# Performance work log

Hardware: AMD Instinct MI355X
Metric: run time of the kernel (lower is better)

The kernel has to match this reference:

```python
import jax, jax.numpy as jnp
import numpy as np

B, N, DIN, DM, NH = 8, 2048, 256, 256, 4
DK = DM // NH


def setup_inputs() -> dict:
    key = jax.random.key(0)
    ks = jax.random.split(key, 8)
    x = jax.random.normal(ks[0], (B, N, DIN), dtype=jnp.float32)
    # contiguous valid ranges per sample (padding on both ends), matching
    # the module's assumption that torch.where(mask)[0][0]/[−1] define a span
    starts = jax.random.randint(ks[1], (B,), 0, N // 8)
    lens = jax.random.randint(ks[2], (B,), N // 2, N - N // 8)
    pos = jnp.arange(N)
    attention_mask = ((pos[None, :] >= starts[:, None])
                      & (pos[None, :] < starts[:, None] + lens[:, None])).astype(jnp.int32)
    s = 0.02
    Wq = jax.random.normal(ks[3], (DIN, DM), jnp.float32) * s
    Wk = jax.random.normal(ks[4], (DIN, DM), jnp.float32) * s
    Wv = jax.random.normal(ks[5], (DIN, DM), jnp.float32) * s
    Wo = jax.random.normal(ks[6], (DM, DM), jnp.float32) * s
    bq = jnp.zeros((DM,), jnp.float32)
    bk = jnp.zeros((DM,), jnp.float32)
    bv = jnp.zeros((DM,), jnp.float32)
    bo = jnp.zeros((DM,), jnp.float32)
    return {"x": x, "attention_mask": attention_mask,
            "Wq": Wq, "bq": bq, "Wk": Wk, "bk": bk,
            "Wv": Wv, "bv": bv, "Wo": Wo, "bo": bo}


def reference(x, attention_mask, Wq, bq, Wk, bk, Wv, bv, Wo, bo):
    b, n, _ = x.shape
    nh, dk = NH, DK
    scale = 1.0 / np.sqrt(dk)
    q = (x @ Wq + bq).reshape(b, n, nh, dk).transpose(0, 2, 1, 3)  # [b,h,n,dk]
    k = (x @ Wk + bk).reshape(b, n, nh, dk).transpose(0, 2, 1, 3)
    v = (x @ Wv + bv).reshape(b, n, nh, dk).transpose(0, 2, 1, 3)
    dist = jnp.einsum('bhid,bhjd->bhij', q, k) * scale  # [b,h,n,n]

    # Vectorized equivalent of the per-sample python-loop mask:
    # start = first True index; end = last True index (torch slice start:end
    # is EXCLUSIVE of the last valid position -- preserved faithfully).
    m = attention_mask.astype(bool)
    pos = jnp.arange(n)
    start = jnp.argmax(m, axis=1)                      # [b]
    end = n - 1 - jnp.argmax(m[:, ::-1], axis=1)       # [b] last True index
    valid = (pos[None, :] >= start[:, None]) & (pos[None, :] < end[:, None])  # [b,n]
    bias = jnp.where(valid[:, :, None] & valid[:, None, :], 0.0, -1e10)       # [b,n,n]

    dist = jax.nn.softmax(dist + bias[:, None, :, :], axis=-1)
    att = jnp.einsum('bhij,bhjd->bhid', dist, v)       # [b,h,n,dk]
    att = att.transpose(0, 2, 1, 3).reshape(b, n, nh * dk)
    return att @ Wo + bo
```

## Files before the change

kernel.cpp:

```cpp
#include <hip/hip_runtime.h>
#include <hip/hip_bf16.h>
#include <math.h>

namespace {
constexpr int Bb  = 8;
constexpr int Nn  = 2048;
constexpr int DIN_ = 256;
constexpr int DM_  = 256;
constexpr int NH_  = 4;
constexpr int DK_  = 64;
constexpr int BH_  = Bb * NH_;
constexpr float SCALE = 0.125f;
}

typedef __attribute__((ext_vector_type(8))) _Float16 half8;
typedef __attribute__((ext_vector_type(2))) __fp16 fp16x2;
typedef __attribute__((ext_vector_type(4))) float f32x4;

static __device__ __forceinline__ unsigned pkrtz_u32(float a, float b) {
    union { fp16x2 h; unsigned u; } u;
    u.h = __builtin_amdgcn_cvt_pkrtz(a, b);
    return u.u;
}

static __device__ __forceinline__ half8 h8_from_u32x4(unsigned w0, unsigned w1,
                                                      unsigned w2, unsigned w3) {
    union { unsigned u[4]; half8 h; } u;
    u.u[0] = w0; u.u[1] = w1; u.u[2] = w2; u.u[3] = w3;
    return u.h;
}

__global__ __launch_bounds__(256) void prep_kernel(
    const int* __restrict__ mask, int* __restrict__ bounds,
    const float* __restrict__ x, _Float16* __restrict__ xh,
    const float* __restrict__ W0, const float* __restrict__ W1,
    const float* __restrict__ W2, const float* __restrict__ W3,
    _Float16* __restrict__ T0, _Float16* __restrict__ T1,
    _Float16* __restrict__ T2, _Float16* __restrict__ T3)
{
    const int bid = blockIdx.x;
    const int tid = threadIdx.x;
    if (bid < 8) {
        const int b = bid;
        __shared__ int smin[256], smax[256];
        int lmin = Nn, lmax = -1;
        for (int i = tid; i < Nn; i += 256) {
            if (mask[b * Nn + i]) {
                if (i < lmin) lmin = i;
                if (i > lmax) lmax = i;
            }
        }
        smin[tid] = lmin; smax[tid] = lmax;
        __syncthreads();
        for (int s = 128; s > 0; s >>= 1) {
            if (tid < s) {
                smin[tid] = min(smin[tid], smin[tid + s]);
                smax[tid] = max(smax[tid], smax[tid + s]);
            }
            __syncthreads();
        }
        if (tid == 0) { bounds[b * 2] = smin[0]; bounds[b * 2 + 1] = smax[0]; }
    } else if (bid < 8 + 2048) {
        const size_t i = ((size_t)(bid - 8) * 256 + tid) * 8;
        float4 v0 = *(const float4*)&x[i];
        float4 v1 = *(const float4*)&x[i + 4];
        _Float16 h[8];
        h[0]=(_Float16)v0.x; h[1]=(_Float16)v0.y; h[2]=(_Float16)v0.z; h[3]=(_Float16)v0.w;
        h[4]=(_Float16)v1.x; h[5]=(_Float16)v1.y; h[6]=(_Float16)v1.z; h[7]=(_Float16)v1.w;
        *(uint4*)&xh[i] = *(const uint4*)h;
    } else {
        const int lin = bid - 2056;
        const int wsel = lin >> 6;
        const float* W; _Float16* T;
        switch (wsel) {
            case 0: W = W0; T = T0; break;
            case 1: W = W1; T = T1; break;
            case 2: W = W2; T = T2; break;
            default: W = W3; T = T3; break;
        }
        const int idx = (lin & 63) * 256 + tid;
        const int n = idx & 255;
        const int k0 = (idx >> 8) << 2;
        _Float16 h4[4];
        #pragma unroll
        for (int j = 0; j < 4; ++j) h4[j] = (_Float16)W[(size_t)(k0 + j) * 256 + n];
        *(uint2*)&T[(size_t)n * 256 + k0] = *(const uint2*)h4;
    }
}

__global__ __launch_bounds__(256) void qkv_mfma(
    const _Float16* __restrict__ xh,
    const _Float16* __restrict__ Wtq, const float* __restrict__ bq,
    const _Float16* __restrict__ Wtk, const float* __restrict__ bk,
    const _Float16* __restrict__ Wtv, const float* __restrict__ bv,
    _Float16* __restrict__ Qh, _Float16* __restrict__ Kh, _Float16* __restrict__ Vt)
{
    const int z = blockIdx.z;
    const _Float16* Wt; const float* bias;
    if (z == 0)      { Wt = Wtq; bias = bq; }
    else if (z == 1) { Wt = Wtk; bias = bk; }
    else             { Wt = Wtv; bias = bv; }

    const int m0 = blockIdx.x * 128;
    const int n0 = blockIdx.y * 64;
    const int tid = threadIdx.x;
    const int w = tid >> 6, lane = tid & 63;
    const int a = lane & 15, g = lane >> 4;
    const int mb = m0 + 32 * w;

    f32x4 d0[4] = {{0,0,0,0},{0,0,0,0},{0,0,0,0},{0,0,0,0}};
    f32x4 d1[4] = {{0,0,0,0},{0,0,0,0},{0,0,0,0},{0,0,0,0}};

    const _Float16* A0 = xh + (size_t)(mb + a) * 256 + 8 * g;
    const _Float16* A1 = xh + (size_t)(mb + 16 + a) * 256 + 8 * g;
    const _Float16* Wr0 = Wt + (size_t)(n0 +  0 + a) * 256 + 8 * g;
    const _Float16* Wr1 = Wt + (size_t)(n0 + 16 + a) * 256 + 8 * g;
    const _Float16* Wr2 = Wt + (size_t)(n0 + 32 + a) * 256 + 8 * g;
    const _Float16* Wr3 = Wt + (size_t)(n0 + 48 + a) * 256 + 8 * g;

    #pragma unroll
    for (int kc = 0; kc < 8; ++kc) {
        const half8 af0 = *(const half8*)(A0 + 32 * kc);
        const half8 af1 = *(const half8*)(A1 + 32 * kc);
        const half8 b0 = *(const half8*)(Wr0 + 32 * kc);
        const half8 b1 = *(const half8*)(Wr1 + 32 * kc);
        const half8 b2 = *(const half8*)(Wr2 + 32 * kc);
        const half8 b3 = *(const half8*)(Wr3 + 32 * kc);
        d0[0] = __builtin_amdgcn_mfma_f32_16x16x32_f16(af0, b0, d0[0], 0,0,0);
        d1[0] = __builtin_amdgcn_mfma_f32_16x16x32_f16(af1, b0, d1[0], 0,0,0);
        d0[1] = __builtin_amdgcn_mfma_f32_16x16x32_f16(af0, b1, d0[1], 0,0,0);
        d1[1] = __builtin_amdgcn_mfma_f32_16x16x32_f16(af1, b1, d1[1], 0,0,0);
        d0[2] = __builtin_amdgcn_mfma_f32_16x16x32_f16(af0, b2, d0[2], 0,0,0);
        d1[2] = __builtin_amdgcn_mfma_f32_16x16x32_f16(af1, b2, d1[2], 0,0,0);
        d0[3] = __builtin_amdgcn_mfma_f32_16x16x32_f16(af0, b3, d0[3], 0,0,0);
        d1[3] = __builtin_amdgcn_mfma_f32_16x16x32_f16(af1, b3, d1[3], 0,0,0);
    }

    #pragma unroll
    for (int t = 0; t < 2; ++t) {
        const int mrow = mb + 16 * t + 4 * g;
        #pragma unroll
        for (int nf = 0; nf < 4; ++nf) {
            const f32x4 dv = t == 0 ? d0[nf] : d1[nf];
            const int n = n0 + 16 * nf + a;
            const float bs = bias[n];
            const int bh = (mrow >> 11) * NH_ + (n >> 6);
            const int dk = n & 63;
            if (z < 2) {
                _Float16* out = z ? Kh : Qh;
                #pragma unroll
                for (int r = 0; r < 4; ++r) {
                    const int tok = (mrow + r) & 2047;
                    out[((size_t)bh * Nn + tok) * DK_ + dk] = (_Float16)(dv[r] + bs);
                }
            } else {
                const int tok = mrow & 2047;
                uint2 pk;
                pk.x = pkrtz_u32(dv[0] + bs, dv[1] + bs);
                pk.y = pkrtz_u32(dv[2] + bs, dv[3] + bs);
                *(uint2*)&Vt[((size_t)bh * DK_ + dk) * Nn + tok] = pk;
            }
        }
    }
}

__global__ __launch_bounds__(256) void colmean_kernel(const _Float16* __restrict__ Vt,
                                                      float* __restrict__ cm) {
    const int bh = blockIdx.x;
    const int t = threadIdx.x;
    const int d = t >> 2, part = t & 3;
    const _Float16* src = Vt + ((size_t)bh * DK_ + d) * Nn + part * 512;
    float s = 0.f;
    for (int i = 0; i < 512; i += 8) {
        half8 v = *(const half8*)(src + i);
        #pragma unroll
        for (int j = 0; j < 8; ++j) s += (float)v[j];
    }
    __shared__ float red[64][4];
    red[d][part] = s;
    __syncthreads();
    if (part == 0)
        cm[bh * DK_ + d] = (red[d][0] + red[d][1] + red[d][2] + red[d][3]) * (1.0f / 2048.0f);
}

__global__ __launch_bounds__(256) void flash_mfma(
    const _Float16* __restrict__ Q, const _Float16* __restrict__ K,
    const _Float16* __restrict__ Vt, const int* __restrict__ bounds,
    const float* __restrict__ cm, _Float16* __restrict__ att)
{
    const int bid = blockIdx.x;
    const int xcd = bid & 7;
    const int rest = bid >> 3;
    const int qb  = rest & 31;
    const int bh  = (xcd << 2) | (rest >> 5);
    const int b  = bh >> 2, h = bh & 3;
    const int q0 = qb * 64;
    const int tid  = threadIdx.x;
    const int w    = tid >> 6;
    const int lane = tid & 63;
    const int a = lane & 15, g = lane >> 4;
    const int start = bounds[2 * b], endv = bounds[2 * b + 1];

    __shared__ __align__(16) _Float16 kfr[2][8][512];
    __shared__ __align__(16) _Float16 vfr[2][8][512];

    const float* cmb = cm + bh * DK_;
    _Float16* attb = att + ((size_t)b * Nn) * DM_ + h * DK_;

    if (q0 + 63 < start || q0 >= endv) {
        #pragma unroll
        for (int td = 0; td < 4; ++td) {
            const _Float16 cmv = (_Float16)cmb[16 * td + a];
            #pragma unroll
            for (int r = 0; r < 4; ++r) {
                const int qr = q0 + 16 * w + 4 * g + r;
                attb[(size_t)qr * DM_ + 16 * td + a] = cmv;
            }
        }
        return;
    }

    const _Float16* Qb = Q  + (size_t)bh * Nn * DK_;
    const _Float16* Kb = K  + (size_t)bh * Nn * DK_;
    const _Float16* Vb = Vt + (size_t)bh * DK_ * Nn;

    const int qrow = q0 + 16 * w + a;
    const half8 qf0 = *(const half8*)&Qb[(size_t)qrow * DK_ + 8 * g];
    const half8 qf1 = *(const half8*)&Qb[(size_t)qrow * DK_ + 32 + 8 * g];

    float l_i = 0.0f;
    f32x4 o0 = {0.f,0.f,0.f,0.f}, o1 = {0.f,0.f,0.f,0.f};
    f32x4 o2 = {0.f,0.f,0.f,0.f}, o3 = {0.f,0.f,0.f,0.f};

#define STAGE(cbuf, kt_) do {                                                        \
        _Pragma("unroll")                                                            \
        for (int ff = 0; ff < 2; ++ff) {                                             \
            const int f  = 2 * w + ff;                                               \
            const int tt = f >> 1, cc = f & 1;                                       \
            const _Float16* ks = &Kb[(size_t)((kt_) + 16 * tt + a) * DK_ + 32 * cc + 8 * g]; \
            __builtin_amdgcn_global_load_lds(                                        \
                (const __attribute__((address_space(1))) void*)ks,                   \
                (__attribute__((address_space(3))) void*)&kfr[cbuf][f][0], 16, 0, 0);\
            const _Float16* vs = &Vb[(size_t)(16 * tt + a) * Nn + (kt_) + 32 * cc + 8 * g]; \
            __builtin_amdgcn_global_load_lds(                                        \
                (const __attribute__((address_space(1))) void*)vs,                   \
                (__attribute__((address_space(3))) void*)&vfr[cbuf][f][0], 16, 0, 0);\
        }                                                                            \
    } while (0)

    const int lo = (start >> 6) * 64;
    int c = 0;
    STAGE(0, lo);

    for (int kt = lo; kt < endv; kt += 64) {
        const int nxt = kt + 64;
        if (nxt < endv) {
            STAGE(c ^ 1, nxt);
            asm volatile("s_waitcnt vmcnt(4)" ::: "memory");
        } else {
            asm volatile("s_waitcnt vmcnt(0)" ::: "memory");
        }
        __builtin_amdgcn_s_barrier();

        const _Float16* kf = &kfr[c][0][0];
        const _Float16* vf = &vfr[c][0][0];

        f32x4 st0 = {0.f,0.f,0.f,0.f}, st1 = {0.f,0.f,0.f,0.f};
        f32x4 st2 = {0.f,0.f,0.f,0.f}, st3 = {0.f,0.f,0.f,0.f};
        st0 = __builtin_amdgcn_mfma_f32_16x16x32_f16(*(const half8*)&kf[0*512 + lane*8], qf0, st0, 0,0,0);
        st0 = __builtin_amdgcn_mfma_f32_16x16x32_f16(*(const half8*)&kf[1*512 + lane*8], qf1, st0, 0,0,0);
        st1 = __builtin_amdgcn_mfma_f32_16x16x32_f16(*(const half8*)&kf[2*512 + lane*8], qf0, st1, 0,0,0);
        st1 = __builtin_amdgcn_mfma_f32_16x16x32_f16(*(const half8*)&kf[3*512 + lane*8], qf1, st1, 0,0,0);
        st2 = __builtin_amdgcn_mfma_f32_16x16x32_f16(*(const half8*)&kf[4*512 + lane*8], qf0, st2, 0,0,0);
        st2 = __builtin_amdgcn_mfma_f32_16x16x32_f16(*(const half8*)&kf[5*512 + lane*8], qf1, st2, 0,0,0);
        st3 = __builtin_amdgcn_mfma_f32_16x16x32_f16(*(const half8*)&kf[6*512 + lane*8], qf0, st3, 0,0,0);
        st3 = __builtin_amdgcn_mfma_f32_16x16x32_f16(*(const half8*)&kf[7*512 + lane*8], qf1, st3, 0,0,0);

        float pv[4][4];
        float rsum = 0.0f;
        const bool edge = (kt < start) || (kt + 64 > endv);
        if (edge) {
            #pragma unroll
            for (int t = 0; t < 4; ++t) {
                const f32x4 sv = (t == 0) ? st0 : (t == 1) ? st1 : (t == 2) ? st2 : st3;
                #pragma unroll
                for (int r = 0; r < 4; ++r) {
                    const int col = kt + 16 * t + 4 * g + r;
                    const bool ok = (col >= start) && (col < endv);
                    const float e = ok ? __expf(sv[r] * SCALE) : 0.0f;
                    pv[t][r] = e;
                    rsum += e;
                }
            }
        } else {
            #pragma unroll
            for (int t = 0; t < 4; ++t) {
                const f32x4 sv = (t == 0) ? st0 : (t == 1) ? st1 : (t == 2) ? st2 : st3;
                #pragma unroll
                for (int r = 0; r < 4; ++r) {
                    const float e = __expf(sv[r] * SCALE);
                    pv[t][r] = e;
                    rsum += e;
                }
            }
        }
        rsum += __shfl_xor(rsum, 16, 64);
        rsum += __shfl_xor(rsum, 32, 64);
        l_i += rsum;

        unsigned pk[4][2];
        #pragma unroll
        for (int t = 0; t < 4; ++t) {
            pk[t][0] = pkrtz_u32(pv[t][0], pv[t][1]);
            pk[t][1] = pkrtz_u32(pv[t][2], pv[t][3]);
        }
        const int gsel = g >> 1;
        unsigned aw[2][4];
        #pragma unroll
        for (int cq = 0; cq < 2; ++cq) {
            #pragma unroll
            for (int wd = 0; wd < 4; ++wd) {
                const int srcLane = a + 16 * (2 * (g & 1) + (wd >> 1));
                const int lo2 = __shfl((int)pk[2 * cq    ][wd & 1], srcLane, 64);
                const int hi2 = __shfl((int)pk[2 * cq + 1][wd & 1], srcLane, 64);
                aw[cq][wd] = (unsigned)(gsel ? hi2 : lo2);
            }
        }
        const half8 pa0 = h8_from_u32x4(aw[0][0], aw[0][1], aw[0][2], aw[0][3]);
        const half8 pa1 = h8_from_u32x4(aw[1][0], aw[1][1], aw[1][2], aw[1][3]);

        o0 = __builtin_amdgcn_mfma_f32_16x16x32_f16(pa0, *(const half8*)&vf[0*512 + lane*8], o0, 0,0,0);
        o0 = __builtin_amdgcn_mfma_f32_16x16x32_f16(pa1, *(const half8*)&vf[1*512 + lane*8], o0, 0,0,0);
        o1 = __builtin_amdgcn_mfma_f32_16x16x32_f16(pa0, *(const half8*)&vf[2*512 + lane*8], o1, 0,0,0);
        o1 = __builtin_amdgcn_mfma_f32_16x16x32_f16(pa1, *(const half8*)&vf[3*512 + lane*8], o1, 0,0,0);
        o2 = __builtin_amdgcn_mfma_f32_16x16x32_f16(pa0, *(const half8*)&vf[4*512 + lane*8], o2, 0,0,0);
        o2 = __builtin_amdgcn_mfma_f32_16x16x32_f16(pa1, *(const half8*)&vf[5*512 + lane*8], o2, 0,0,0);
        o3 = __builtin_amdgcn_mfma_f32_16x16x32_f16(pa0, *(const half8*)&vf[6*512 + lane*8], o3, 0,0,0);
        o3 = __builtin_amdgcn_mfma_f32_16x16x32_f16(pa1, *(const half8*)&vf[7*512 + lane*8], o3, 0,0,0);

        asm volatile("" ::: "memory");
        __builtin_amdgcn_s_barrier();
        c ^= 1;
    }
#undef STAGE

    const float inv = 1.0f / l_i;
    const float ir0 = __shfl(inv, 4 * g + 0, 64);
    const float ir1 = __shfl(inv, 4 * g + 1, 64);
    const float ir2 = __shfl(inv, 4 * g + 2, 64);
    const float ir3 = __shfl(inv, 4 * g + 3, 64);

    #pragma unroll
    for (int td = 0; td < 4; ++td) {
        const f32x4 ov = (td == 0) ? o0 : (td == 1) ? o1 : (td == 2) ? o2 : o3;
        const float cmv = cmb[16 * td + a];
        const float irs[4] = {ir0, ir1, ir2, ir3};
        #pragma unroll
        for (int r = 0; r < 4; ++r) {
            const int qr = q0 + 16 * w + 4 * g + r;
            const bool valid = (qr >= start) && (qr < endv);
            const float val = valid ? ov[r] * irs[r] : cmv;
            attb[(size_t)qr * DM_ + 16 * td + a] = (_Float16)val;
        }
    }
}

__global__ __launch_bounds__(256) void proj_mfma(
    const _Float16* __restrict__ A, const _Float16* __restrict__ Wt,
    const float* __restrict__ bias, float* __restrict__ out)
{
    const int m0 = blockIdx.x * 128;
    const int n0 = blockIdx.y * 64;
    const int tid = threadIdx.x;
    const int w = tid >> 6, lane = tid & 63;
    const int a = lane & 15, g = lane >> 4;
    const int mb = m0 + 32 * w;

    f32x4 d0[4] = {{0,0,0,0},{0,0,0,0},{0,0,0,0},{0,0,0,0}};
    f32x4 d1[4] = {{0,0,0,0},{0,0,0,0},{0,0,0,0},{0,0,0,0}};

    const _Float16* A0 = A + (size_t)(mb + a) * 256 + 8 * g;
    const _Float16* A1 = A + (size_t)(mb + 16 + a) * 256 + 8 * g;
    const _Float16* Wr0 = Wt + (size_t)(n0 +  0 + a) * 256 + 8 * g;
    const _Float16* Wr1 = Wt + (size_t)(n0 + 16 + a) * 256 + 8 * g;
    const _Float16* Wr2 = Wt + (size_t)(n0 + 32 + a) * 256 + 8 * g;
    const _Float16* Wr3 = Wt + (size_t)(n0 + 48 + a) * 256 + 8 * g;

    #pragma unroll
    for (int kc = 0; kc < 8; ++kc) {
        const half8 af0 = *(const half8*)(A0 + 32 * kc);
        const half8 af1 = *(const half8*)(A1 + 32 * kc);
        const half8 b0 = *(const half8*)(Wr0 + 32 * kc);
        const half8 b1 = *(const half8*)(Wr1 + 32 * kc);
        const half8 b2 = *(const half8*)(Wr2 + 32 * kc);
        const half8 b3 = *(const half8*)(Wr3 + 32 * kc);
        d0[0] = __builtin_amdgcn_mfma_f32_16x16x32_f16(af0, b0, d0[0], 0,0,0);
        d1[0] = __builtin_amdgcn_mfma_f32_16x16x32_f16(af1, b0, d1[0], 0,0,0);
        d0[1] = __builtin_amdgcn_mfma_f32_16x16x32_f16(af0, b1, d0[1], 0,0,0);
        d1[1] = __builtin_amdgcn_mfma_f32_16x16x32_f16(af1, b1, d1[1], 0,0,0);
        d0[2] = __builtin_amdgcn_mfma_f32_16x16x32_f16(af0, b2, d0[2], 0,0,0);
        d1[2] = __builtin_amdgcn_mfma_f32_16x16x32_f16(af1, b2, d1[2], 0,0,0);
        d0[3] = __builtin_amdgcn_mfma_f32_16x16x32_f16(af0, b3, d0[3], 0,0,0);
        d1[3] = __builtin_amdgcn_mfma_f32_16x16x32_f16(af1, b3, d1[3], 0,0,0);
    }

    #pragma unroll
    for (int t = 0; t < 2; ++t) {
        const int mrow = mb + 16 * t + 4 * g;
        #pragma unroll
        for (int nf = 0; nf < 4; ++nf) {
            const f32x4 dv = t == 0 ? d0[nf] : d1[nf];
            const int n = n0 + 16 * nf + a;
            const float bs = bias[n];
            #pragma unroll
            for (int r = 0; r < 4; ++r)
                out[(size_t)(mrow + r) * DM_ + n] = dv[r] + bs;
        }
    }
}

extern "C" void kernel_launch(void* const* d_in, const int* in_sizes, int n_in,
                              void* d_out, int out_size, void* d_ws, size_t ws_size,
                              hipStream_t stream)
{
    const float* x    = (const float*)d_in[0];
    const int*   mask = (const int*)d_in[1];
    const float* Wq   = (const float*)d_in[2];
    const float* bq   = (const float*)d_in[3];
    const float* Wk   = (const float*)d_in[4];
    const float* bk   = (const float*)d_in[5];
    const float* Wv   = (const float*)d_in[6];
    const float* bv   = (const float*)d_in[7];
    const float* Wo   = (const float*)d_in[8];
    const float* bo   = (const float*)d_in[9];
    float* out = (float*)d_out;

    char* ws = (char*)d_ws;
    size_t off = 0;
    int* bounds = (int*)ws;                 off += 256;
    float* cmv  = (float*)(ws + off);       off += (size_t)BH_ * DK_ * sizeof(float);
    off = (off + 255) & ~(size_t)255;
    const size_t h16_bytes = (size_t)BH_ * Nn * DK_ * sizeof(_Float16);
    _Float16* xh  = (_Float16*)(ws + off); off += h16_bytes;
    _Float16* Qh  = (_Float16*)(ws + off); off += h16_bytes;
    _Float16* Kh  = (_Float16*)(ws + off); off += h16_bytes;
    _Float16* Vt  = (_Float16*)(ws + off); off += h16_bytes;
    _Float16* ath = (_Float16*)(ws + off); off += h16_bytes;
    _Float16* Wtq = (_Float16*)(ws + off); off += 256 * 256 * sizeof(_Float16);
    _Float16* Wtk = (_Float16*)(ws + off); off += 256 * 256 * sizeof(_Float16);
    _Float16* Wtv = (_Float16*)(ws + off); off += 256 * 256 * sizeof(_Float16);
    _Float16* Wto = (_Float16*)(ws + off); off += 256 * 256 * sizeof(_Float16);

    prep_kernel<<<2312, 256, 0, stream>>>(mask, bounds, x, xh,
                                          Wq, Wk, Wv, Wo, Wtq, Wtk, Wtv, Wto);

    dim3 g1(Bb * Nn / 128, DM_ / 64, 3);
    qkv_mfma<<<g1, 256, 0, stream>>>(xh, Wtq, bq, Wtk, bk, Wtv, bv, Qh, Kh, Vt);

    colmean_kernel<<<BH_, 256, 0, stream>>>(Vt, cmv);

    flash_mfma<<<1024, 256, 0, stream>>>(Qh, Kh, Vt, bounds, cmv, ath);

    dim3 g3(Bb * Nn / 128, DM_ / 64);
    proj_mfma<<<g3, 256, 0, stream>>>(ath, Wto, bo, out);
}
```

Measured before the change: 208.9 us.

## Split attention key range in two and merge partial results in combine kernel

Flash attention now splits each query block's key range into two halves handled by separate workgroups, doubling the grid. Each writes unnormalised fp16 partial outputs and row sums, and a new combine kernel adds them, normalises, and fills padded rows with the column mean. The goal is more parallelism and better load balance across CUs. The cost is an extra kernel launch and the extra global traffic for the partial buffers. It also risks lower precision, since unnormalised partial sums are stored in fp16.

```diff
diff --git a/kernel.cpp b/kernel.cpp
--- a/kernel.cpp
+++ b/kernel.cpp
@@ -186,13 +186,15 @@
 __global__ __launch_bounds__(256) void flash_mfma(
     const _Float16* __restrict__ Q, const _Float16* __restrict__ K,
     const _Float16* __restrict__ Vt, const int* __restrict__ bounds,
-    const float* __restrict__ cm, _Float16* __restrict__ att)
+    _Float16* __restrict__ Oh, float* __restrict__ lw)
 {
     const int bid = blockIdx.x;
     const int xcd = bid & 7;
     const int rest = bid >> 3;
     const int qb  = rest & 31;
-    const int bh  = (xcd << 2) | (rest >> 5);
+    const int j   = (rest >> 5) & 3;
+    const int s   = rest >> 7;
+    const int bh  = j * 8 + xcd;
     const int b  = bh >> 2, h = bh & 3;
     const int q0 = qb * 64;
     const int tid  = threadIdx.x;
@@ -201,24 +203,10 @@
     const int a = lane & 15, g = lane >> 4;
     const int start = bounds[2 * b], endv = bounds[2 * b + 1];
 
+    if (q0 + 63 < start || q0 >= endv) return;
+
     __shared__ __align__(16) _Float16 kfr[2][8][512];
     __shared__ __align__(16) _Float16 vfr[2][8][512];
-
-    const float* cmb = cm + bh * DK_;
-    _Float16* attb = att + ((size_t)b * Nn) * DM_ + h * DK_;
-
-    if (q0 + 63 < start || q0 >= endv) {
-        #pragma unroll
-        for (int td = 0; td < 4; ++td) {
-            const _Float16 cmv = (_Float16)cmb[16 * td + a];
-            #pragma unroll
-            for (int r = 0; r < 4; ++r) {
-                const int qr = q0 + 16 * w + 4 * g + r;
-                attb[(size_t)qr * DM_ + 16 * td + a] = cmv;
-            }
-        }
-        return;
-    }
 
     const _Float16* Qb = Q  + (size_t)bh * Nn * DK_;
     const _Float16* Kb = K  + (size_t)bh * Nn * DK_;
@@ -248,120 +236,167 @@
         }                                                                            \
     } while (0)
 
-    const int lo = (start >> 6) * 64;
-    int c = 0;
-    STAGE(0, lo);
-
-    for (int kt = lo; kt < endv; kt += 64) {
-        const int nxt = kt + 64;
-        if (nxt < endv) {
-            STAGE(c ^ 1, nxt);
-            asm volatile("s_waitcnt vmcnt(4)" ::: "memory");
-        } else {
-            asm volatile("s_waitcnt vmcnt(0)" ::: "memory");
-        }
-        __builtin_amdgcn_s_barrier();
-
-        const _Float16* kf = &kfr[c][0][0];
-        const _Float16* vf = &vfr[c][0][0];
-
-        f32x4 st0 = {0.f,0.f,0.f,0.f}, st1 = {0.f,0.f,0.f,0.f};
-        f32x4 st2 = {0.f,0.f,0.f,0.f}, st3 = {0.f,0.f,0.f,0.f};
-        st0 = __builtin_amdgcn_mfma_f32_16x16x32_f16(*(const half8*)&kf[0*512 + lane*8], qf0, st0, 0,0,0);
-        st0 = __builtin_amdgcn_mfma_f32_16x16x32_f16(*(const half8*)&kf[1*512 + lane*8], qf1, st0, 0,0,0);
-        st1 = __builtin_amdgcn_mfma_f32_16x16x32_f16(*(const half8*)&kf[2*512 + lane*8], qf0, st1, 0,0,0);
-        st1 = __builtin_amdgcn_mfma_f32_16x16x32_f16(*(const half8*)&kf[3*512 + lane*8], qf1, st1, 0,0,0);
-        st2 = __builtin_amdgcn_mfma_f32_16x16x32_f16(*(const half8*)&kf[4*512 + lane*8], qf0, st2, 0,0,0);
-        st2 = __builtin_amdgcn_mfma_f32_16x16x32_f16(*(const half8*)&kf[5*512 + lane*8], qf1, st2, 0,0,0);
-        st3 = __builtin_amdgcn_mfma_f32_16x16x32_f16(*(const half8*)&kf[6*512 + lane*8], qf0, st3, 0,0,0);
-        st3 = __builtin_amdgcn_mfma_f32_16x16x32_f16(*(const half8*)&kf[7*512 + lane*8], qf1, st3, 0,0,0);
-
-        float pv[4][4];
-        float rsum = 0.0f;
-        const bool edge = (kt < start) || (kt + 64 > endv);
-        if (edge) {
+    const int t0 = start >> 6, t1 = (endv + 63) >> 6;
+    const int nt = t1 - t0;
+    const int n0t = (nt + 1) >> 1;
+    const int ts = (s == 0) ? t0 : t0 + n0t;
+    const int te = (s == 0) ? t0 + n0t : t1;
+
+    if (ts < te) {
+        const int lo = ts * 64, hiend = te * 64;
+        int c = 0;
+        STAGE(0, lo);
+
+        for (int kt = lo; kt < hiend; kt += 64) {
+            const int nxt = kt + 64;
+            if (nxt < hiend) {
+                STAGE(c ^ 1, nxt);
+                asm volatile("s_waitcnt vmcnt(4)" ::: "memory");
+            } else {
+                asm volatile("s_waitcnt vmcnt(0)" ::: "memory");
+            }
+            __builtin_amdgcn_s_barrier();
+
+            const _Float16* kf = &kfr[c][0][0];
+            const _Float16* vf = &vfr[c][0][0];
+
+            f32x4 st0 = {0.f,0.f,0.f,0.f}, st1 = {0.f,0.f,0.f,0.f};
+            f32x4 st2 = {0.f,0.f,0.f,0.f}, st3 = {0.f,0.f,0.f,0.f};
+            st0 = __builtin_amdgcn_mfma_f32_16x16x32_f16(*(const half8*)&kf[0*512 + lane*8], qf0, st0, 0,0,0);
+            st0 = __builtin_amdgcn_mfma_f32_16x16x32_f16(*(const half8*)&kf[1*512 + lane*8], qf1, st0, 0,0,0);
+            st1 = __builtin_amdgcn_mfma_f32_16x16x32_f16(*(const half8*)&kf[2*512 + lane*8], qf0, st1, 0,0,0);
+            st1 = __builtin_amdgcn_mfma_f32_16x16x32_f16(*(const half8*)&kf[3*512 + lane*8], qf1, st1, 0,0,0);
+            st2 = __builtin_amdgcn_mfma_f32_16x16x32_f16(*(const half8*)&kf[4*512 + lane*8], qf0, st2, 0,0,0);
+            st2 = __builtin_amdgcn_mfma_f32_16x16x32_f16(*(const half8*)&kf[5*512 + lane*8], qf1, st2, 0,0,0);
+            st3 = __builtin_amdgcn_mfma_f32_16x16x32_f16(*(const half8*)&kf[6*512 + lane*8], qf0, st3, 0,0,0);
+            st3 = __builtin_amdgcn_mfma_f32_16x16x32_f16(*(const half8*)&kf[7*512 + lane*8], qf1, st3, 0,0,0);
+
+            float pv[4][4];
+            float rsum = 0.0f;
+            const bool edge = (kt < start) || (kt + 64 > endv);
+            if (edge) {
+                #pragma unroll
+                for (int t = 0; t < 4; ++t) {
+                    const f32x4 sv = (t == 0) ? st0 : (t == 1) ? st1 : (t == 2) ? st2 : st3;
+                    #pragma unroll
+                    for (int r = 0; r < 4; ++r) {
+                        const int col = kt + 16 * t + 4 * g + r;
+                        const bool ok = (col >= start) && (col < endv);
+                        const float e = ok ? __expf(sv[r] * SCALE) : 0.0f;
+                        pv[t][r] = e;
+                        rsum += e;
+                    }
+                }
+            } else {
+                #pragma unroll
+                for (int t = 0; t < 4; ++t) {
+                    const f32x4 sv = (t == 0) ? st0 : (t == 1) ? st1 : (t == 2) ? st2 : st3;
+                    #pragma unroll
+                    for (int r = 0; r < 4; ++r) {
+                        const float e = __expf(sv[r] * SCALE);
+                        pv[t][r] = e;
+                        rsum += e;
+                    }
+                }
+            }
+            rsum += __shfl_xor(rsum, 16, 64);
+            rsum += __shfl_xor(rsum, 32, 64);
+            l_i += rsum;
+
+            unsigned pk[4][2];
             #pragma unroll
             for (int t = 0; t < 4; ++t) {
-                const f32x4 sv = (t == 0) ? st0 : (t == 1) ? st1 : (t == 2) ? st2 : st3;
+                pk[t][0] = pkrtz_u32(pv[t][0], pv[t][1]);
+                pk[t][1] = pkrtz_u32(pv[t][2], pv[t][3]);
+            }
+            const int gsel = g >> 1;
+            unsigned aw[2][4];
+            #pragma unroll
+            for (int cq = 0; cq < 2; ++cq) {
                 #pragma unroll
-                for (int r = 0; r < 4; ++r) {
-                    const int col = kt + 16 * t + 4 * g + r;
-                    const bool ok = (col >= start) && (col < endv);
-                    const float e = ok ? __expf(sv[r] * SCALE) : 0.0f;
-                    pv[t][r] = e;
-                    rsum += e;
+                for (int wd = 0; wd < 4; ++wd) {
+                    const int srcLane = a + 16 * (2 * (g & 1) + (wd >> 1));
+                    const int lo2 = __shfl((int)pk[2 * cq    ][wd & 1], srcLane, 64);
+                    const int hi2 = __shfl((int)pk[2 * cq + 1][wd & 1], srcLane, 64);
+                    aw[cq][wd] = (unsigned)(gsel ? hi2 : lo2);
                 }
             }
-        } else {
-            #pragma unroll
-            for (int t = 0; t < 4; ++t) {
-                const f32x4 sv = (t == 0) ? st0 : (t == 1) ? st1 : (t == 2) ? st2 : st3;
-                #pragma unroll
-                for (int r = 0; r < 4; ++r) {
-                    const float e = __expf(sv[r] * SCALE);
-                    pv[t][r] = e;
-                    rsum += e;
-                }
-            }
-        }
-        rsum += __shfl_xor(rsum, 16, 64);
-        rsum += __shfl_xor(rsum, 32, 64);
-        l_i += rsum;
-
-        unsigned pk[4][2];
-        #pragma unroll
-        for (int t = 0; t < 4; ++t) {
-            pk[t][0] = pkrtz_u32(pv[t][0], pv[t][1]);
-            pk[t][1] = pkrtz_u32(pv[t][2], pv[t][3]);
-        }
-        const int gsel = g >> 1;
-        unsigned aw[2][4];
-        #pragma unroll
-        for (int cq = 0; cq < 2; ++cq) {
-            #pragma unroll
-            for (int wd = 0; wd < 4; ++wd) {
-                const int srcLane = a + 16 * (2 * (g & 1) + (wd >> 1));
-                const int lo2 = __shfl((int)pk[2 * cq    ][wd & 1], srcLane, 64);
-                const int hi2 = __shfl((int)pk[2 * cq + 1][wd & 1], srcLane, 64);
-                aw[cq][wd] = (unsigned)(gsel ? hi2 : lo2);
-            }
-        }
-        const half8 pa0 = h8_from_u32x4(aw[0][0], aw[0][1], aw[0][2], aw[0][3]);
-        const half8 pa1 = h8_from_u32x4(aw[1][0], aw[1][1], aw[1][2], aw[1][3]);
-
-        o0 = __builtin_amdgcn_mfma_f32_16x16x32_f16(pa0, *(const half8*)&vf[0*512 + lane*8], o0, 0,0,0);
-        o0 = __builtin_amdgcn_mfma_f32_16x16x32_f16(pa1, *(const half8*)&vf[1*512 + lane*8], o0, 0,0,0);
-        o1 = __builtin_amdgcn_mfma_f32_16x16x32_f16(pa0, *(const half8*)&vf[2*512 + lane*8], o1, 0,0,0);
-        o1 = __builtin_amdgcn_mfma_f32_16x16x32_f16(pa1, *(const half8*)&vf[3*512 + lane*8], o1, 0,0,0);
-        o2 = __builtin_amdgcn_mfma_f32_16x16x32_f16(pa0, *(const half8*)&vf[4*512 + lane*8], o2, 0,0,0);
-        o2 = __builtin_amdgcn_mfma_f32_16x16x32_f16(pa1, *(const half8*)&vf[5*512 + lane*8], o2, 0,0,0);
-        o3 = __builtin_amdgcn_mfma_f32_16x16x32_f16(pa0, *(const half8*)&vf[6*512 + lane*8], o3, 0,0,0);
-        o3 = __builtin_amdgcn_mfma_f32_16x16x32_f16(pa1, *(const half8*)&vf[7*512 + lane*8], o3, 0,0,0);
-
-        asm volatile("" ::: "memory");
-        __builtin_amdgcn_s_barrier();
-        c ^= 1;
+            const half8 pa0 = h8_from_u32x4(aw[0][0], aw[0][1], aw[0][2], aw[0][3]);
+            const half8 pa1 = h8_from_u32x4(aw[1][0], aw[1][1], aw[1][2], aw[1][3]);
+
+            o0 = __builtin_amdgcn_mfma_f32_16x16x32_f16(pa0, *(const half8*)&vf[0*512 + lane*8], o0, 0,0,0);
+            o0 = __builtin_amdgcn_mfma_f32_16x16x32_f16(pa1, *(const half8*)&vf[1*512 + lane*8], o0, 0,0,0);
+            o1 = __builtin_amdgcn_mfma_f32_16x16x32_f16(pa0, *(const half8*)&vf[2*512 + lane*8], o1, 0,0,0);
+            o1 = __builtin_amdgcn_mfma_f32_16x16x32_f16(pa1, *(const half8*)&vf[3*512 + lane*8], o1, 0,0,0);
+            o2 = __builtin_amdgcn_mfma_f32_16x16x32_f16(pa0, *(const half8*)&vf[4*512 + lane*8], o2, 0,0,0);
+            o2 = __builtin_amdgcn_mfma_f32_16x16x32_f16(pa1, *(const half8*)&vf[5*512 + lane*8], o2, 0,0,0);
+            o3 = __builtin_amdgcn_mfma_f32_16x16x32_f16(pa0, *(const half8*)&vf[6*512 + lane*8], o3, 0,0,0);
+            o3 = __builtin_amdgcn_mfma_f32_16x16x32_f16(pa1, *(const half8*)&vf[7*512 + lane*8], o3, 0,0,0);
+
+            asm volatile("" ::: "memory");
+            __builtin_amdgcn_s_barrier();
+            c ^= 1;
+        }
     }
 #undef STAGE
 
-    const float inv = 1.0f / l_i;
-    const float ir0 = __shfl(inv, 4 * g + 0, 64);
-    const float ir1 = __shfl(inv, 4 * g + 1, 64);
-    const float ir2 = __shfl(inv, 4 * g + 2, 64);
-    const float ir3 = __shfl(inv, 4 * g + 3, 64);
-
+    const size_t half = (size_t)Bb * Nn * DM_;
+    _Float16* ob = Oh + (size_t)s * half + ((size_t)b * Nn) * DM_ + h * DK_;
     #pragma unroll
     for (int td = 0; td < 4; ++td) {
         const f32x4 ov = (td == 0) ? o0 : (td == 1) ? o1 : (td == 2) ? o2 : o3;
-        const float cmv = cmb[16 * td + a];
-        const float irs[4] = {ir0, ir1, ir2, ir3};
         #pragma unroll
         for (int r = 0; r < 4; ++r) {
             const int qr = q0 + 16 * w + 4 * g + r;
-            const bool valid = (qr >= start) && (qr < endv);
-            const float val = valid ? ov[r] * irs[r] : cmv;
-            attb[(size_t)qr * DM_ + 16 * td + a] = (_Float16)val;
-        }
+            ob[(size_t)qr * DM_ + 16 * td + a] = (_Float16)ov[r];
+        }
+    }
+    if (g == 0) {
+        const int tok = q0 + 16 * w + a;
+        lw[(size_t)s * BH_ * Nn + (size_t)bh * Nn + tok] = l_i;
+    }
+}
+
+__global__ __launch_bounds__(256) void combine_kernel(
+    const _Float16* __restrict__ Oh, const float* __restrict__ lw,
+    const int* __restrict__ bounds, const float* __restrict__ cm,
+    _Float16* __restrict__ att)
+{
+    const int b  = blockIdx.y;
+    const int q0 = blockIdx.x * 64;
+    const int t  = threadIdx.x;
+    const int row = q0 + (t >> 2);
+    const int h   = t & 3;
+    const int c0  = h * 64;
+    const int start = bounds[2 * b], endv = bounds[2 * b + 1];
+    const bool valid = (row >= start) && (row < endv);
+
+    const size_t half = (size_t)Bb * Nn * DM_;
+    const size_t rowoff = ((size_t)b * Nn + row) * DM_ + c0;
+
+    float inv = 0.0f;
+    if (valid) {
+        const int bh = b * NH_ + h;
+        const float l0 = lw[(size_t)bh * Nn + row];
+        const float l1 = lw[(size_t)BH_ * Nn + (size_t)bh * Nn + row];
+        inv = 1.0f / (l0 + l1);
+    }
+
+    #pragma unroll
+    for (int jj = 0; jj < 64; jj += 8) {
+        _Float16 o[8];
+        if (valid) {
+            half8 a0 = *(const half8*)&Oh[rowoff + jj];
+            half8 a1 = *(const half8*)&Oh[half + rowoff + jj];
+            #pragma unroll
+            for (int k = 0; k < 8; ++k)
+                o[k] = (_Float16)(((float)a0[k] + (float)a1[k]) * inv);
+        } else {
+            #pragma unroll
+            for (int k = 0; k < 8; ++k)
+                o[k] = (_Float16)cm[b * DM_ + c0 + jj + k];
+        }
+        *(uint4*)&att[rowoff + jj] = *(const uint4*)o;
     }
 }
 
@@ -440,11 +475,13 @@
     int* bounds = (int*)ws;                 off += 256;
     float* cmv  = (float*)(ws + off);       off += (size_t)BH_ * DK_ * sizeof(float);
     off = (off + 255) & ~(size_t)255;
+    float* lw   = (float*)(ws + off);       off += (size_t)2 * BH_ * Nn * sizeof(float);
     const size_t h16_bytes = (size_t)BH_ * Nn * DK_ * sizeof(_Float16);
     _Float16* xh  = (_Float16*)(ws + off); off += h16_bytes;
     _Float16* Qh  = (_Float16*)(ws + off); off += h16_bytes;
     _Float16* Kh  = (_Float16*)(ws + off); off += h16_bytes;
     _Float16* Vt  = (_Float16*)(ws + off); off += h16_bytes;
+    _Float16* Oh  = (_Float16*)(ws + off); off += 2 * h16_bytes;
     _Float16* ath = (_Float16*)(ws + off); off += h16_bytes;
     _Float16* Wtq = (_Float16*)(ws + off); off += 256 * 256 * sizeof(_Float16);
     _Float16* Wtk = (_Float16*)(ws + off); off += 256 * 256 * sizeof(_Float16);
@@ -459,7 +496,10 @@
 
     colmean_kernel<<<BH_, 256, 0, stream>>>(Vt, cmv);
 
-    flash_mfma<<<1024, 256, 0, stream>>>(Qh, Kh, Vt, bounds, cmv, ath);
+    flash_mfma<<<2048, 256, 0, stream>>>(Qh, Kh, Vt, bounds, Oh, lw);
+
+    dim3 gc(Nn / 64, Bb);
+    combine_kernel<<<gc, 256, 0, stream>>>(Oh, lw, bounds, cmv, ath);
 
     dim3 g3(Bb * Nn / 128, DM_ / 64);
     proj_mfma<<<g3, 256, 0, stream>>>(ath, Wto, bo, out);
```

Result: no change. 208.3 us (-0.3%).
